# Optimization experiments

Hardware: AMD Instinct MI355X
Metric: run time of the kernel (lower is better)

Reference implementation:

```python
import jax, jax.numpy as jnp
import numpy as np

N_NODES = 50000


def setup_inputs() -> dict:
    key = jax.random.key(0)
    k1, k2, k3 = jax.random.split(key, 3)
    B, E, HS = 4, 800000, 16
    H = jax.random.normal(k1, (B, N_NODES, HS, HS), dtype=jnp.float32)
    edge_index = jax.random.randint(k2, (B, E, 2), 0, N_NODES, dtype=jnp.int32)
    edge_weight = jax.random.normal(k3, (B, E), dtype=jnp.float32)
    node_idx = jnp.arange(N_NODES, dtype=jnp.int32)  # identity id->row map
    return {"H": H, "edge_index": edge_index, "edge_weight": edge_weight,
            "node_idx": node_idx}


def reference(H, edge_index, edge_weight, node_idx):
    # Original builds adj[b, node1, node2] = w, krons with eye(h_size), and does
    # sparse.mm(H_adj, H). Blockwise this is exactly:
    #   out[b, u, :, :] = sum_{edges (u, v) in batch b} w * H[b, v, :, :]
    # node_idx maps raw node ids to rows; with arange it is the identity, so we
    # index by id directly (faithful to torch.where(node_idx == id)).
    inv = jnp.argsort(node_idx)  # id -> row (identity for arange)

    def agg_one(Hb, eb, wb):
        src_rows = inv[eb[:, 1]]  # node2: gathered neighbor
        dst_rows = inv[eb[:, 0]]  # node1: aggregation target
        msgs = Hb[src_rows] * wb[:, None, None]  # (E, hs, hs)
        return jax.ops.segment_sum(msgs, dst_rows, num_segments=N_NODES)

    return jax.vmap(agg_one)(H, edge_index, edge_weight)
```

## Files before the change

### kernel.cpp

```cpp
#include <hip/hip_runtime.h>


constexpr int ROW = 256;
constexpr int CAP = 32;
constexpr int OVFCAP = 262144;

typedef _Float16 half4 __attribute__((ext_vector_type(4)));
typedef float fvec4 __attribute__((ext_vector_type(4)));

static __device__ inline float h2f_bits(unsigned short u) {
    _Float16 h; __builtin_memcpy(&h, &u, 2); return (float)h;
}

__global__ void k_init(const int* __restrict__ nidx, int* __restrict__ inv,
                       int* __restrict__ zbuf, int nz, int N) {
    int i = blockIdx.x * blockDim.x + threadIdx.x;
    if (i < N) inv[nidx[i]] = i;
    if (i < nz) zbuf[i] = 0;
}

__global__ __launch_bounds__(256)
void k_prep(const fvec4* __restrict__ H, half4* __restrict__ Hh, size_t n4, int cvtBlocks,
            int scatBlocks,
            const unsigned long long* __restrict__ ei, const float* __restrict__ ew,
            const int* __restrict__ inv, int* __restrict__ cursor,
            unsigned* __restrict__ edges, int* __restrict__ ovfcnt,
            uint2* __restrict__ ovf, int B, int E, int N) {
    if ((int)blockIdx.x < cvtBlocks) {
        size_t stride = (size_t)cvtBlocks * 256;
        for (size_t i = (size_t)blockIdx.x * 256 + threadIdx.x; i < n4; i += stride) {
            fvec4 v = __builtin_nontemporal_load(&H[i]);
            half4 o;
            o.x = (_Float16)v.x; o.y = (_Float16)v.y;
            o.z = (_Float16)v.z; o.w = (_Float16)v.w;
            Hh[i] = o;
        }
    } else {
        int total = B * E;
        int stride = scatBlocks * 256;
        for (int idx = ((int)blockIdx.x - cvtBlocks) * 256 + (int)threadIdx.x;
             idx < total; idx += stride) {
            unsigned long long pq = __builtin_nontemporal_load(&ei[idx]);
            int b = idx / E;
            int dst = inv[(int)(pq & 0xFFFFFFFFull)];
            int src = inv[(int)(pq >> 32)];
            float w = __builtin_nontemporal_load(&ew[idx]);
            _Float16 hw = (_Float16)w;
            unsigned short wb; __builtin_memcpy(&wb, &hw, 2);
            unsigned rec = (unsigned)(unsigned short)src | ((unsigned)wb << 16);
            size_t sidx = (size_t)b * N + dst;
            int pos = atomicAdd(&cursor[sidx], 1);
            if (pos < CAP) {
                __builtin_nontemporal_store(rec, &edges[sidx * CAP + pos]);
            } else {
                int op = atomicAdd(ovfcnt, 1);
                if (op < OVFCAP)
                    ovf[op] = make_uint2(((unsigned)b << 16) | (unsigned)dst, rec);
            }
        }
    }
}

__device__ inline void fma4(fvec4& acc, float w, half4 h) {
    acc.x += w * (float)h.x; acc.y += w * (float)h.y;
    acc.z += w * (float)h.z; acc.w += w * (float)h.w;
}

__global__ __launch_bounds__(256)
void k_agg_gap(const _Float16* __restrict__ Hh, const int* __restrict__ cursor,
               const unsigned* __restrict__ edges, float* __restrict__ out,
               int B, int N, int xpb) {
    int lane = threadIdx.x & 63;
    int wid = threadIdx.x >> 6;
    int b, grp;
    if (xpb > 0) {
        int bi = blockIdx.x;
        int xcd = bi & 7;
        b = xcd / xpb;
        grp = (bi >> 3) * xpb + (xcd % xpb);
    } else {
        b = blockIdx.y;
        grp = blockIdx.x;
    }
    int node = grp * 4 + wid;
    if (node >= N) return;
    size_t sidx = (size_t)b * N + node;
    int deg = cursor[sidx];
    if (deg > CAP) deg = CAP;
    const unsigned* seg = edges + sidx * CAP;
    unsigned rec = 0;
    if (lane < deg) rec = __builtin_nontemporal_load(&seg[lane]);
    const half4* Hb = (const half4*)(Hh + (size_t)b * N * ROW);
    fvec4 acc = {0.f, 0.f, 0.f, 0.f};
    int j = 0;
    for (; j + 8 <= deg; j += 8) {
        int sv[8]; float wv[8];
#pragma unroll
        for (int u = 0; u < 8; ++u) {
            unsigned r = __shfl(rec, j + u);
            sv[u] = (int)(r & 0xFFFFu);
            wv[u] = h2f_bits((unsigned short)(r >> 16));
        }
        half4 hv[8];
#pragma unroll
        for (int u = 0; u < 8; ++u) hv[u] = Hb[(size_t)sv[u] * 64 + lane];
#pragma unroll
        for (int u = 0; u < 8; ++u) fma4(acc, wv[u], hv[u]);
    }
    if (j + 4 <= deg) {
        int sv[4]; float wv[4];
#pragma unroll
        for (int u = 0; u < 4; ++u) {
            unsigned r = __shfl(rec, j + u);
            sv[u] = (int)(r & 0xFFFFu);
            wv[u] = h2f_bits((unsigned short)(r >> 16));
        }
        half4 hv[4];
#pragma unroll
        for (int u = 0; u < 4; ++u) hv[u] = Hb[(size_t)sv[u] * 64 + lane];
#pragma unroll
        for (int u = 0; u < 4; ++u) fma4(acc, wv[u], hv[u]);
        j += 4;
    }
    for (; j < deg; ++j) {
        unsigned r = __shfl(rec, j);
        half4 h = Hb[(size_t)(r & 0xFFFFu) * 64 + lane];
        fma4(acc, h2f_bits((unsigned short)(r >> 16)), h);
    }
    __builtin_nontemporal_store(acc, (fvec4*)out + (sidx * 64 + lane));
}

__global__ __launch_bounds__(256)
void k_ovf(const _Float16* __restrict__ Hh, const int* __restrict__ ovfcnt,
           const uint2* __restrict__ ovf, float* __restrict__ out, int N) {
    int lane = threadIdx.x & 63;
    int wv = (blockIdx.x * 256 + (int)threadIdx.x) >> 6;
    int nw = gridDim.x * 4;
    int count = *ovfcnt;
    if (count > OVFCAP) count = OVFCAP;
    for (int i = wv; i < count; i += nw) {
        uint2 v = ovf[i];
        int b = (int)(v.x >> 16);
        int dst = (int)(v.x & 0xFFFFu);
        int src = (int)(v.y & 0xFFFFu);
        float w = h2f_bits((unsigned short)(v.y >> 16));
        half4 h = ((const half4*)(Hh + (size_t)b * N * ROW))[(size_t)src * 64 + lane];
        float* op = out + ((size_t)b * N + dst) * ROW + lane * 4;
        atomicAdd(op + 0, w * (float)h.x);
        atomicAdd(op + 1, w * (float)h.y);
        atomicAdd(op + 2, w * (float)h.z);
        atomicAdd(op + 3, w * (float)h.w);
    }
}

__global__ void k_zero_f32(float* __restrict__ p, size_t n) {
    size_t i = (size_t)blockIdx.x * blockDim.x + threadIdx.x;
    if (i < n) p[i] = 0.f;
}

__global__ void k_atomic_agg(const float* __restrict__ H, const int* __restrict__ ei,
                             const float* __restrict__ ew, const int* __restrict__ inv,
                             float* __restrict__ out, int B, int E, int N) {
    int lane = threadIdx.x & 63;
    int widx = (blockIdx.x * blockDim.x + threadIdx.x) >> 6;
    int total = B * E;
    if (widx >= total) return;
    int b = widx / E;
    int d = ei[(size_t)widx * 2];
    int s = ei[(size_t)widx * 2 + 1];
    if (inv) { d = inv[d]; s = inv[s]; }
    float w = ew[widx];
    const float4* hp = (const float4*)(H + ((size_t)b * N + s) * ROW);
    float4 h = hp[lane];
    float* op = out + ((size_t)b * N + d) * ROW + lane * 4;
    atomicAdd(op + 0, w * h.x);
    atomicAdd(op + 1, w * h.y);
    atomicAdd(op + 2, w * h.z);
    atomicAdd(op + 3, w * h.w);
}

static inline size_t alignup(size_t x) { return (x + 255) & ~(size_t)255; }

extern "C" void kernel_launch(void* const* d_in, const int* in_sizes, int n_in,
                              void* d_out, int out_size, void* d_ws, size_t ws_size,
                              hipStream_t stream) {
    const float* H = (const float*)d_in[0];
    const int* ei = (const int*)d_in[1];
    const float* ew = (const float*)d_in[2];
    const int* nidx = (const int*)d_in[3];
    float* out = (float*)d_out;

    int N = in_sizes[3];
    int B = in_sizes[0] / (N * ROW);
    int E = in_sizes[2] / B;
    int total = B * E;
    size_t nH = (size_t)B * N * ROW;
    char* w0 = (char*)d_ws;

    size_t o_inv = 0;
    size_t o_cur = alignup(o_inv + (size_t)N * 4);
    size_t ncur = (size_t)B * N + 1;
    size_t o_ovf = alignup(o_cur + ncur * 4);
    size_t o_seg = alignup(o_ovf + (size_t)OVFCAP * 8);
    size_t o_hh = alignup(o_seg + (size_t)B * N * CAP * 4);
    size_t req = o_hh + nH * 2;

    if (ws_size >= req && N <= 65535 && B <= 65535) {
        int* g_inv = (int*)(w0 + o_inv);
        int* g_cursor = (int*)(w0 + o_cur);
        int* g_ovfcnt = g_cursor + (size_t)B * N;
        uint2* g_ovf = (uint2*)(w0 + o_ovf);
        unsigned* g_edges = (unsigned*)(w0 + o_seg);
        _Float16* Hh = (_Float16*)(w0 + o_hh);

        int nz = (int)ncur;
        int ninit = max(N, nz);
        k_init<<<(ninit + 255) / 256, 256, 0, stream>>>(nidx, g_inv, g_cursor, nz, N);
        int cvtBlocks = 896, scatBlocks = 1152;
        k_prep<<<cvtBlocks + scatBlocks, 256, 0, stream>>>(
            (const fvec4*)H, (half4*)Hh, nH / 4, cvtBlocks, scatBlocks,
            (const unsigned long long*)ei, ew, g_inv, g_cursor, g_edges,
            g_ovfcnt, g_ovf, B, E, N);

        int groupsPerB = (N + 3) / 4;
        int xpb = (B > 0 && 8 % B == 0) ? 8 / B : 0;
        bool can_swz = xpb > 0 && (groupsPerB % xpb) == 0 &&
                       (((size_t)groupsPerB * B) % 8) == 0;
        if (can_swz) {
            k_agg_gap<<<groupsPerB * B, 256, 0, stream>>>(
                Hh, g_cursor, g_edges, out, B, N, xpb);
        } else {
            dim3 ag(groupsPerB, B);
            k_agg_gap<<<ag, 256, 0, stream>>>(Hh, g_cursor, g_edges, out, B, N, 0);
        }
        k_ovf<<<256, 256, 0, stream>>>(Hh, g_ovfcnt, g_ovf, out, N);
        return;
    }

    int* finv = nullptr;
    if (ws_size >= (size_t)N * sizeof(int)) {
        finv = (int*)d_ws;
        k_init<<<(N + 255) / 256, 256, 0, stream>>>(nidx, finv, finv, 0, N);
    }
    size_t on = (size_t)out_size;
    k_zero_f32<<<(int)((on + 255) / 256), 256, 0, stream>>>(out, on);
    int blocks = (total * 64 + 255) / 256;
    k_atomic_agg<<<blocks, 256, 0, stream>>>(H, ei, ew, finv, out, B, E, N);
}
```

Baseline: 400.4 us.

## Bucket edges by destination range before building per-node adjacency lists

```diff
diff --git a/kernel.cpp b/kernel.cpp
--- a/kernel.cpp
+++ b/kernel.cpp
@@ -3,7 +3,10 @@
 
 constexpr int ROW = 256;
 constexpr int CAP = 32;
-constexpr int OVFCAP = 262144;
+constexpr int NBKT = 256;
+constexpr int BKCAP = 8192;
+constexpr int OVFCAP = 65536;
+constexpr int MAXBSZ = 512;
 
 typedef _Float16 half4 __attribute__((ext_vector_type(4)));
 typedef float fvec4 __attribute__((ext_vector_type(4)));
@@ -20,12 +23,173 @@
 }
 
 __global__ __launch_bounds__(256)
-void k_prep(const fvec4* __restrict__ H, half4* __restrict__ Hh, size_t n4, int cvtBlocks,
-            int scatBlocks,
-            const unsigned long long* __restrict__ ei, const float* __restrict__ ew,
-            const int* __restrict__ inv, int* __restrict__ cursor,
-            unsigned* __restrict__ edges, int* __restrict__ ovfcnt,
-            uint2* __restrict__ ovf, int B, int E, int N) {
+void k_prep1(const fvec4* __restrict__ H, half4* __restrict__ Hh, size_t n4,
+             const unsigned long long* __restrict__ ei, const float* __restrict__ ew,
+             const int* __restrict__ inv, int* __restrict__ bktcnt,
+             unsigned long long* __restrict__ bkt, int B, int E, int N, int bucketSz) {
+    size_t tid0 = (size_t)blockIdx.x * 256 + threadIdx.x;
+    size_t stride = (size_t)gridDim.x * 256;
+    long long total = (long long)B * E;
+    for (long long idx = (long long)tid0; idx < total; idx += (long long)stride) {
+        int i = (int)idx;
+        unsigned long long pq = __builtin_nontemporal_load(&ei[i]);
+        int b = i / E;
+        int dst = inv[(int)(pq & 0xFFFFFFFFull)];
+        int src = inv[(int)(pq >> 32)];
+        float w = __builtin_nontemporal_load(&ew[i]);
+        _Float16 hw = (_Float16)w;
+        unsigned short wb; __builtin_memcpy(&wb, &hw, 2);
+        unsigned rec = (unsigned)(unsigned short)src | ((unsigned)wb << 16);
+        int q = dst / bucketSz;
+        int bq = b * NBKT + q;
+        int pos = atomicAdd(&bktcnt[bq], 1);
+        if (pos < BKCAP) {
+            unsigned long long e = ((unsigned long long)rec << 32) | (unsigned)dst;
+            __builtin_nontemporal_store(e, &bkt[(size_t)bq * BKCAP + pos]);
+        }
+    }
+    for (size_t i = tid0; i < n4; i += stride) {
+        fvec4 v = __builtin_nontemporal_load(&H[i]);
+        half4 o;
+        o.x = (_Float16)v.x; o.y = (_Float16)v.y;
+        o.z = (_Float16)v.z; o.w = (_Float16)v.w;
+        Hh[i] = o;
+    }
+}
+
+__global__ __launch_bounds__(256)
+void k_pass2(const unsigned long long* __restrict__ bkt, const int* __restrict__ bktcnt,
+             unsigned* __restrict__ edges, int* __restrict__ cursor,
+             int* __restrict__ ovfcnt, uint2* __restrict__ ovf,
+             int B, int N, int bucketSz) {
+    __shared__ int lcur[MAXBSZ];
+    int bq = blockIdx.x;
+    int b = bq / NBKT;
+    int q = bq % NBKT;
+    int base = q * bucketSz;
+    int nloc = min(bucketSz, N - base);
+    if (nloc <= 0) return;
+    for (int t = threadIdx.x; t < nloc; t += 256) lcur[t] = 0;
+    __syncthreads();
+    int cnt = bktcnt[bq];
+    if (cnt > BKCAP) cnt = BKCAP;
+    for (int i = threadIdx.x; i < cnt; i += 256) {
+        unsigned long long e = bkt[(size_t)bq * BKCAP + i];
+        int dst = (int)(e & 0xFFFFFFFFull);
+        unsigned rec = (unsigned)(e >> 32);
+        int pos = atomicAdd(&lcur[dst - base], 1);
+        if (pos < CAP) {
+            __builtin_nontemporal_store(rec, &edges[((size_t)b * N + dst) * CAP + pos]);
+        } else {
+            int op = atomicAdd(ovfcnt, 1);
+            if (op < OVFCAP)
+                ovf[op] = make_uint2(((unsigned)b << 16) | (unsigned)dst, rec);
+        }
+    }
+    __syncthreads();
+    for (int t = threadIdx.x; t < nloc; t += 256)
+        cursor[(size_t)b * N + base + t] = lcur[t];
+}
+
+__device__ inline void fma4(fvec4& acc, float w, half4 h) {
+    acc.x += w * (float)h.x; acc.y += w * (float)h.y;
+    acc.z += w * (float)h.z; acc.w += w * (float)h.w;
+}
+
+__global__ __launch_bounds__(256)
+void k_agg_gap(const _Float16* __restrict__ Hh, const int* __restrict__ cursor,
+               const unsigned* __restrict__ edges, float* __restrict__ out,
+               int B, int N, int xpb) {
+    int lane = threadIdx.x & 63;
+    int wid = threadIdx.x >> 6;
+    int b, grp;
+    if (xpb > 0) {
+        int bi = blockIdx.x;
+        int xcd = bi & 7;
+        b = xcd / xpb;
+        grp = (bi >> 3) * xpb + (xcd % xpb);
+    } else {
+        b = blockIdx.y;
+        grp = blockIdx.x;
+    }
+    int node = grp * 4 + wid;
+    if (node >= N) return;
+    size_t sidx = (size_t)b * N + node;
+    int deg = cursor[sidx];
+    if (deg > CAP) deg = CAP;
+    const unsigned* seg = edges + sidx * CAP;
+    unsigned rec = 0;
+    if (lane < deg) rec = __builtin_nontemporal_load(&seg[lane]);
+    const half4* Hb = (const half4*)(Hh + (size_t)b * N * ROW);
+    fvec4 acc = {0.f, 0.f, 0.f, 0.f};
+    int j = 0;
+    for (; j + 8 <= deg; j += 8) {
+        int sv[8]; float wv[8];
+#pragma unroll
+        for (int u = 0; u < 8; ++u) {
+            unsigned r = __shfl(rec, j + u);
+            sv[u] = (int)(r & 0xFFFFu);
+            wv[u] = h2f_bits((unsigned short)(r >> 16));
+        }
+        half4 hv[8];
+#pragma unroll
+        for (int u = 0; u < 8; ++u) hv[u] = Hb[(size_t)sv[u] * 64 + lane];
+#pragma unroll
+        for (int u = 0; u < 8; ++u) fma4(acc, wv[u], hv[u]);
+    }
+    if (j + 4 <= deg) {
+        int sv[4]; float wv[4];
+#pragma unroll
+        for (int u = 0; u < 4; ++u) {
+            unsigned r = __shfl(rec, j + u);
+            sv[u] = (int)(r & 0xFFFFu);
+            wv[u] = h2f_bits((unsigned short)(r >> 16));
+        }
+        half4 hv[4];
+#pragma unroll
+        for (int u = 0; u < 4; ++u) hv[u] = Hb[(size_t)sv[u] * 64 + lane];
+#pragma unroll
+        for (int u = 0; u < 4; ++u) fma4(acc, wv[u], hv[u]);
+        j += 4;
+    }
+    for (; j < deg; ++j) {
+        unsigned r = __shfl(rec, j);
+        half4 h = Hb[(size_t)(r & 0xFFFFu) * 64 + lane];
+        fma4(acc, h2f_bits((unsigned short)(r >> 16)), h);
+    }
+    __builtin_nontemporal_store(acc, (fvec4*)out + (sidx * 64 + lane));
+}
+
+__global__ __launch_bounds__(256)
+void k_ovf(const _Float16* __restrict__ Hh, const int* __restrict__ ovfcnt,
+           const uint2* __restrict__ ovf, float* __restrict__ out, int N) {
+    int lane = threadIdx.x & 63;
+    int wv = (blockIdx.x * 256 + (int)threadIdx.x) >> 6;
+    int nw = gridDim.x * 4;
+    int count = *ovfcnt;
+    if (count > OVFCAP) count = OVFCAP;
+    for (int i = wv; i < count; i += nw) {
+        uint2 v = ovf[i];
+        int b = (int)(v.x >> 16);
+        int dst = (int)(v.x & 0xFFFFu);
+        int src = (int)(v.y & 0xFFFFu);
+        float w = h2f_bits((unsigned short)(v.y >> 16));
+        half4 h = ((const half4*)(Hh + (size_t)b * N * ROW))[(size_t)src * 64 + lane];
+        float* op = out + ((size_t)b * N + dst) * ROW + lane * 4;
+        atomicAdd(op + 0, w * (float)h.x);
+        atomicAdd(op + 1, w * (float)h.y);
+        atomicAdd(op + 2, w * (float)h.z);
+        atomicAdd(op + 3, w * (float)h.w);
+    }
+}
+
+__global__ __launch_bounds__(256)
+void k_prep_rs(const fvec4* __restrict__ H, half4* __restrict__ Hh, size_t n4,
+               int cvtBlocks, int scatBlocks,
+               const unsigned long long* __restrict__ ei, const float* __restrict__ ew,
+               const int* __restrict__ inv, int* __restrict__ cursor,
+               unsigned* __restrict__ edges, int* __restrict__ ovfcnt,
+               uint2* __restrict__ ovf, int B, int E, int N) {
     if ((int)blockIdx.x < cvtBlocks) {
         size_t stride = (size_t)cvtBlocks * 256;
         for (size_t i = (size_t)blockIdx.x * 256 + threadIdx.x; i < n4; i += stride) {
@@ -61,98 +225,6 @@
     }
 }
 
-__device__ inline void fma4(fvec4& acc, float w, half4 h) {
-    acc.x += w * (float)h.x; acc.y += w * (float)h.y;
-    acc.z += w * (float)h.z; acc.w += w * (float)h.w;
-}
-
-__global__ __launch_bounds__(256)
-void k_agg_gap(const _Float16* __restrict__ Hh, const int* __restrict__ cursor,
-               const unsigned* __restrict__ edges, float* __restrict__ out,
-               int B, int N, int xpb) {
-    int lane = threadIdx.x & 63;
-    int wid = threadIdx.x >> 6;
-    int b, grp;
-    if (xpb > 0) {
-        int bi = blockIdx.x;
-        int xcd = bi & 7;
-        b = xcd / xpb;
-        grp = (bi >> 3) * xpb + (xcd % xpb);
-    } else {
-        b = blockIdx.y;
-        grp = blockIdx.x;
-    }
-    int node = grp * 4 + wid;
-    if (node >= N) return;
-    size_t sidx = (size_t)b * N + node;
-    int deg = cursor[sidx];
-    if (deg > CAP) deg = CAP;
-    const unsigned* seg = edges + sidx * CAP;
-    unsigned rec = 0;
-    if (lane < deg) rec = __builtin_nontemporal_load(&seg[lane]);
-    const half4* Hb = (const half4*)(Hh + (size_t)b * N * ROW);
-    fvec4 acc = {0.f, 0.f, 0.f, 0.f};
-    int j = 0;
-    for (; j + 8 <= deg; j += 8) {
-        int sv[8]; float wv[8];
-#pragma unroll
-        for (int u = 0; u < 8; ++u) {
-            unsigned r = __shfl(rec, j + u);
-            sv[u] = (int)(r & 0xFFFFu);
-            wv[u] = h2f_bits((unsigned short)(r >> 16));
-        }
-        half4 hv[8];
-#pragma unroll
-        for (int u = 0; u < 8; ++u) hv[u] = Hb[(size_t)sv[u] * 64 + lane];
-#pragma unroll
-        for (int u = 0; u < 8; ++u) fma4(acc, wv[u], hv[u]);
-    }
-    if (j + 4 <= deg) {
-        int sv[4]; float wv[4];
-#pragma unroll
-        for (int u = 0; u < 4; ++u) {
-            unsigned r = __shfl(rec, j + u);
-            sv[u] = (int)(r & 0xFFFFu);
-            wv[u] = h2f_bits((unsigned short)(r >> 16));
-        }
-        half4 hv[4];
-#pragma unroll
-        for (int u = 0; u < 4; ++u) hv[u] = Hb[(size_t)sv[u] * 64 + lane];
-#pragma unroll
-        for (int u = 0; u < 4; ++u) fma4(acc, wv[u], hv[u]);
-        j += 4;
-    }
-    for (; j < deg; ++j) {
-        unsigned r = __shfl(rec, j);
-        half4 h = Hb[(size_t)(r & 0xFFFFu) * 64 + lane];
-        fma4(acc, h2f_bits((unsigned short)(r >> 16)), h);
-    }
-    __builtin_nontemporal_store(acc, (fvec4*)out + (sidx * 64 + lane));
-}
-
-__global__ __launch_bounds__(256)
-void k_ovf(const _Float16* __restrict__ Hh, const int* __restrict__ ovfcnt,
-           const uint2* __restrict__ ovf, float* __restrict__ out, int N) {
-    int lane = threadIdx.x & 63;
-    int wv = (blockIdx.x * 256 + (int)threadIdx.x) >> 6;
-    int nw = gridDim.x * 4;
-    int count = *ovfcnt;
-    if (count > OVFCAP) count = OVFCAP;
-    for (int i = wv; i < count; i += nw) {
-        uint2 v = ovf[i];
-        int b = (int)(v.x >> 16);
-        int dst = (int)(v.x & 0xFFFFu);
-        int src = (int)(v.y & 0xFFFFu);
-        float w = h2f_bits((unsigned short)(v.y >> 16));
-        half4 h = ((const half4*)(Hh + (size_t)b * N * ROW))[(size_t)src * 64 + lane];
-        float* op = out + ((size_t)b * N + dst) * ROW + lane * 4;
-        atomicAdd(op + 0, w * (float)h.x);
-        atomicAdd(op + 1, w * (float)h.y);
-        atomicAdd(op + 2, w * (float)h.z);
-        atomicAdd(op + 3, w * (float)h.w);
-    }
-}
-
 __global__ void k_zero_f32(float* __restrict__ p, size_t n) {
     size_t i = (size_t)blockIdx.x * blockDim.x + threadIdx.x;
     if (i < n) p[i] = 0.f;
@@ -196,31 +268,45 @@
     int total = B * E;
     size_t nH = (size_t)B * N * ROW;
     char* w0 = (char*)d_ws;
+    int bucketSz = (N + NBKT - 1) / NBKT;
 
     size_t o_inv = 0;
     size_t o_cur = alignup(o_inv + (size_t)N * 4);
-    size_t ncur = (size_t)B * N + 1;
+    size_t ncur = (size_t)B * N + 1 + (size_t)B * NBKT;
     size_t o_ovf = alignup(o_cur + ncur * 4);
     size_t o_seg = alignup(o_ovf + (size_t)OVFCAP * 8);
     size_t o_hh = alignup(o_seg + (size_t)B * N * CAP * 4);
     size_t req = o_hh + nH * 2;
+    size_t bkt_bytes = (size_t)B * NBKT * BKCAP * 8;
+    bool radix_ok = bucketSz <= MAXBSZ && bkt_bytes <= (size_t)out_size * 4;
 
     if (ws_size >= req && N <= 65535 && B <= 65535) {
         int* g_inv = (int*)(w0 + o_inv);
         int* g_cursor = (int*)(w0 + o_cur);
         int* g_ovfcnt = g_cursor + (size_t)B * N;
+        int* g_bktcnt = g_ovfcnt + 1;
         uint2* g_ovf = (uint2*)(w0 + o_ovf);
         unsigned* g_edges = (unsigned*)(w0 + o_seg);
         _Float16* Hh = (_Float16*)(w0 + o_hh);
+        unsigned long long* g_bkt = (unsigned long long*)d_out;
 
         int nz = (int)ncur;
         int ninit = max(N, nz);
         k_init<<<(ninit + 255) / 256, 256, 0, stream>>>(nidx, g_inv, g_cursor, nz, N);
-        int cvtBlocks = 896, scatBlocks = 1152;
-        k_prep<<<cvtBlocks + scatBlocks, 256, 0, stream>>>(
-            (const fvec4*)H, (half4*)Hh, nH / 4, cvtBlocks, scatBlocks,
-            (const unsigned long long*)ei, ew, g_inv, g_cursor, g_edges,
-            g_ovfcnt, g_ovf, B, E, N);
+
+        if (radix_ok) {
+            k_prep1<<<2048, 256, 0, stream>>>(
+                (const fvec4*)H, (half4*)Hh, nH / 4,
+                (const unsigned long long*)ei, ew, g_inv, g_bktcnt, g_bkt,
+                B, E, N, bucketSz);
+            k_pass2<<<B * NBKT, 256, 0, stream>>>(
+                g_bkt, g_bktcnt, g_edges, g_cursor, g_ovfcnt, g_ovf, B, N, bucketSz);
+        } else {
+            k_prep_rs<<<2048, 256, 0, stream>>>(
+                (const fvec4*)H, (half4*)Hh, nH / 4, 896, 1152,
+                (const unsigned long long*)ei, ew, g_inv, g_cursor, g_edges,
+                g_ovfcnt, g_ovf, B, E, N);
+        }
 
         int groupsPerB = (N + 3) / 4;
         int xpb = (B > 0 && 8 % B == 0) ? 8 / B : 0;
```

After: 1.102 ms. 175% more time.
